# Performance work log

Measured on AMD Instinct MI355X. Metric: run time of the kernel, lower is better.

The kernel has to match this reference:

```python
import jax, jax.numpy as jnp
import numpy as np

NLAT, NLON = 256, 512
LMAX, MMAX = 256, 257  # legendre-gauss: lmax=nlat, mmax=nlon//2+1
BATCH, CHAN = 16, 8


def setup_inputs() -> dict:
    key = jax.random.key(0)
    kx, kw = jax.random.split(key)
    # vector field on the sphere: [..., 2 (theta/phi components), nlat, nlon]
    x = jax.random.normal(kx, (BATCH, CHAN, 2, NLAT, NLON), dtype=jnp.float32)
    # precomputed Legendre-derivative quadrature weights [2, mmax, lmax, nlat]
    # (stands in for precompute_dlegpoly * quad weights * 1/(l(l+1)), with weights[1] sign flip folded in)
    weights = 0.02 * jax.random.normal(kw, (2, MMAX, LMAX, NLAT), dtype=jnp.float32)
    return {"x": x, "weights": weights}


def reference(x, weights):
    # forward rfft over longitude, scaled by 2*pi (norm='forward' divides by nlon)
    xf = (2.0 * jnp.pi) * jnp.fft.rfft(x, axis=-1, norm="forward")  # [..., 2, nlat, nfreq] complex
    mmax = weights.shape[1]
    xf = xf[..., :mmax]
    # split vector components and real/imag parts
    xt = xf[..., 0, :, :]  # theta component [..., nlat, mmax]
    xp = xf[..., 1, :, :]  # phi component
    xtr, xti = jnp.real(xt), jnp.imag(xt)
    xpr, xpi = jnp.real(xp), jnp.imag(xp)
    w0 = weights[0]  # [mmax, lmax, nlat]
    w1 = weights[1]

    def contract(a, w):
        # batched per-m matmul: [..., k, m] x [m, l, k] -> [..., l, m]
        return jnp.einsum("...km,mlk->...lm", a, w)

    # spheroidal (component 0) and toroidal (component 1) coefficients
    out0 = (contract(xtr, w0) - contract(xpi, w1)) + 1j * (contract(xti, w0) + contract(xpr, w1))
    out1 = (-contract(xti, w1) - contract(xpr, w0)) + 1j * (contract(xtr, w1) - contract(xpi, w0))
    return jnp.stack([out0, out1], axis=-3)  # [..., 2, lmax, mmax] complex64
```

## Files before the change

### kernel.cpp

```cpp
#include <hip/hip_runtime.h>
#include <hip/hip_bf16.h>
#include <math.h>

#define NLAT 256
#define NLON 512
#define LMAX 256
#define MMAX 257
#define BC   128

#define X_ELEMS 33554432
#define W_ELEMS 33685504
#define W_BYTES (W_ELEMS * 4LL)

#define FM    288
#define F_BYTES  ((size_t)2*FM*512*2)
#define A_BYTES  ((size_t)4*BC*MMAX*NLAT*2)
#define OUTS_BYTES ((size_t)MMAX*2*BC*LMAX*2)

typedef short bf16x8 __attribute__((ext_vector_type(8)));
typedef float f32x4  __attribute__((ext_vector_type(4)));

__device__ __forceinline__ unsigned int bfpack2(float a, float b) {
    unsigned short lo = __builtin_bit_cast(unsigned short, __float2bfloat16(a));
    unsigned short hi = __builtin_bit_cast(unsigned short, __float2bfloat16(b));
    return (unsigned int)lo | ((unsigned int)hi << 16);
}
__device__ __forceinline__ unsigned short bf16bits(float a) {
    return __builtin_bit_cast(unsigned short, __float2bfloat16(a));
}
__device__ __forceinline__ void gload16(const void* g, void* l) {
    __builtin_amdgcn_global_load_lds(
        (const __attribute__((address_space(1))) unsigned int*)g,
        (__attribute__((address_space(3))) unsigned int*)l, 16, 0, 0);
}

__global__ __launch_bounds__(256) void f_init(unsigned short* __restrict__ F)
{
    int mm = blockIdx.x, o = blockIdx.y, t = threadIdx.x;
    const float s = 6.283185307179586f / 512.0f;
    for (int c = 0; c < 2; ++c) {
        int n = t * 2 + c;
        float val = 0.0f;
        if (mm < MMAX) {
            int j = (mm * n) & 511;
            float ang = 6.283185307179586f * (float)j / 512.0f;
            float sn, cs; __sincosf(ang, &sn, &cs);
            val = (o == 0) ? s * cs : -s * sn;
        }
        F[((size_t)o * FM + mm) * 512 + n] =
            __builtin_bit_cast(unsigned short, __float2bfloat16(val));
    }
}

__global__ __launch_bounds__(512, 1) void dft_mfma(const float* __restrict__ x,
                                                   const unsigned short* __restrict__ F,
                                                   unsigned short* __restrict__ aout)
{
    __shared__ __align__(16) unsigned char fl[2][32768];
    unsigned char* xl = (unsigned char*)fl;

    int bcc = blockIdx.x;
    int kh  = blockIdx.y;
    int bc = bcc >> 1, comp = bcc & 1;
    int t = threadIdx.x;
    int wid = t >> 6, lane = t & 63;

    int o = wid >> 2, kt = wid & 3;
    int r15 = lane & 15, hi = lane >> 4;
    int klocal = kt * 16 + r15;
    unsigned braw = (unsigned)klocal * 1024u;
    unsigned bswz = (unsigned)(klocal & 15) << 4;

    bf16x8 barr0[16], barr1[16];
    #pragma unroll
    for (int s = 0; s < 2; ++s) {
        const float* xg = x + ((size_t)bcc * NLAT + kh * 128 + s * 64) * NLON;
        #pragma unroll
        for (int p = 0; p < 8; ++p) {
            int row = wid * 8 + p;
            const float* src = xg + (size_t)row * NLON + lane * 8;
            float4 f0 = *(const float4*)(src);
            float4 f1 = *(const float4*)(src + 4);
            uint4 v;
            v.x = bfpack2(f0.x, f0.y); v.y = bfpack2(f0.z, f0.w);
            v.z = bfpack2(f1.x, f1.y); v.w = bfpack2(f1.z, f1.w);
            unsigned off = ((unsigned)row * 1024u + (unsigned)lane * 16u)
                           ^ ((unsigned)(row & 15) << 4);
            *(uint4*)(xl + off) = v;
        }
        __syncthreads();
        #pragma unroll
        for (int nt = 0; nt < 16; ++nt) {
            unsigned c0 = (unsigned)(nt * 64 + hi * 16);
            bf16x8 v = *(const bf16x8*)(xl + ((braw + c0) ^ bswz));
            if (s == 0) barr0[nt] = v; else barr1[nt] = v;
        }
        __syncthreads();
    }

    const unsigned char* Fb = (const unsigned char*)F;
    unsigned gcol = ((unsigned)lane * 16u);

    #define STAGE_F(buf, mt)                                                  \
        {                                                                     \
            _Pragma("unroll")                                                 \
            for (int p = 0; p < 4; ++p) {                                     \
                int fr = wid * 4 + p;                                         \
                int o2 = fr >> 4, mr = fr & 15;                               \
                size_t grow = (size_t)o2 * FM + (mt) * 16 + mr;               \
                const void* g = Fb + grow * 1024u                             \
                                + (gcol ^ ((unsigned)(fr & 15) << 4));        \
                gload16(g, (unsigned char*)fl[buf] + (unsigned)fr * 1024u);   \
            }                                                                 \
        }

    STAGE_F(0, 0);
    __syncthreads();

    unsigned arow = (unsigned)(o * 16 + r15);
    unsigned abase = arow * 1024u;
    unsigned aswz = (unsigned)r15 << 4;
    unsigned short* ao = aout;
    int v = comp * 2 + o;

    for (int mt = 0; mt < 17; ++mt) {
        int cur = mt & 1;
        if (mt < 16) STAGE_F(cur ^ 1, mt + 1);

        const unsigned char* fb = fl[cur];
        f32x4 accA0 = {0.f,0.f,0.f,0.f}, accA1 = {0.f,0.f,0.f,0.f};
        f32x4 accB0 = {0.f,0.f,0.f,0.f}, accB1 = {0.f,0.f,0.f,0.f};
        #pragma unroll
        for (int nt = 0; nt < 16; nt += 2) {
            unsigned c0 = (unsigned)(nt * 64 + hi * 16);
            bf16x8 a0 = *(const bf16x8*)(fb + ((abase + c0)       ^ aswz));
            bf16x8 a1 = *(const bf16x8*)(fb + ((abase + c0 + 64u) ^ aswz));
            accA0 = __builtin_amdgcn_mfma_f32_16x16x32_bf16(a0, barr0[nt],     accA0, 0, 0, 0);
            accB0 = __builtin_amdgcn_mfma_f32_16x16x32_bf16(a0, barr1[nt],     accB0, 0, 0, 0);
            accA1 = __builtin_amdgcn_mfma_f32_16x16x32_bf16(a1, barr0[nt + 1], accA1, 0, 0, 0);
            accB1 = __builtin_amdgcn_mfma_f32_16x16x32_bf16(a1, barr1[nt + 1], accB1, 0, 0, 0);
        }
        #pragma unroll
        for (int j = 0; j < 4; ++j) {
            accA0[j] += accA1[j];
            accB0[j] += accB1[j];
        }

        #pragma unroll
        for (int j = 0; j < 4; ++j) {
            int mm0 = mt * 16 + hi * 4 + j;
            if (mm0 < MMAX) {
                size_t base = (((size_t)v * BC + bc) * MMAX + mm0) * NLAT + kh * 128;
                ao[base + klocal]      = bf16bits(accA0[j]);
                ao[base + klocal + 64] = bf16bits(accB0[j]);
            }
        }
        __syncthreads();
    }
    #undef STAGE_F
}

template <int MODE>
__global__ __launch_bounds__(1024, 1) void contract_mfma(const unsigned short* __restrict__ a,
                                                         const float* __restrict__ w,
                                                         void* __restrict__ outv)
{
    __shared__ __align__(16) unsigned char Ab[2][16384];
    __shared__ __align__(16) unsigned char Bb[2][40960];
    int m  = blockIdx.x;
    int t = threadIdx.x;
    int wid = t >> 6, lane = t & 63;
    int o = wid >> 3, h = (wid >> 2) & 1, q = wid & 3;
    int r15 = lane & 15, hi = lane >> 4;

    f32x4 acc[4][4] = {};

    int pl  = t >> 9;
    int bcr = (t >> 2) & 127;
    int ch4 = t & 3;
    int lB  = t >> 2;
    int chB = t & 3;

    #define STAGE_A(buf, kt)                                                    \
        {                                                                       \
            int ph_ = (kt) >> 3;                                                \
            int k0_ = ((kt) & 7) * 32;                                          \
            int vsel = (pl == 0) ? (ph_ ? 3 : 0) : (ph_ ? 1 : 2);               \
            const void* g = a + (((size_t)vsel * BC + bcr) * MMAX + m) * NLAT   \
                              + k0_ + (ch4 ^ (bcr & 3)) * 8;                    \
            gload16(g, Ab[buf] + wid * 1024);                                   \
        }

    float4 wreg0, wreg1;
    #define WLOAD(kt)                                                           \
        {                                                                       \
            int ph_ = (kt) >> 3;                                                \
            int k0_ = ((kt) & 7) * 32;                                          \
            const float* wp = w + (((size_t)ph_ * MMAX + m) * LMAX + lB) * NLAT \
                                + k0_ + chB * 8;                                \
            wreg0 = *(const float4*)(wp);                                       \
            wreg1 = *(const float4*)(wp + 4);                                   \
        }
    #define BWRITE(buf)                                                         \
        {                                                                       \
            uint4 vv;                                                           \
            vv.x = bfpack2(wreg0.x, wreg0.y); vv.y = bfpack2(wreg0.z, wreg0.w); \
            vv.z = bfpack2(wreg1.x, wreg1.y); vv.w = bfpack2(wreg1.z, wreg1.w); \
            *(uint4*)(Bb[buf] + lB * 80 + chB * 16) = vv;                       \
            uint4 vn;                                                           \
            vn.x = vv.x ^ 0x80008000u; vn.y = vv.y ^ 0x80008000u;               \
            vn.z = vv.z ^ 0x80008000u; vn.w = vv.w ^ 0x80008000u;               \
            *(uint4*)(Bb[buf] + 20480 + lB * 80 + chB * 16) = vn;               \
        }

    STAGE_A(0, 0);
    WLOAD(0);
    __syncthreads();
    BWRITE(0);

    for (int kt2 = 0; kt2 < 16; ++kt2) {
        int cur = kt2 & 1;
        if (kt2 < 15) WLOAD(kt2 + 1);
        __syncthreads();
        if (kt2 < 15) STAGE_A(cur ^ 1, kt2 + 1);

        const unsigned char* bb = Bb[cur] + ((o == 0 && kt2 >= 8) ? 20480 : 0);
        const unsigned char* ab = Ab[cur];
        bf16x8 bfr[4];
        #pragma unroll
        for (int lt = 0; lt < 4; ++lt)
            bfr[lt] = *(const bf16x8*)(bb + (q * 64 + lt * 16 + r15) * 80 + hi * 16);
        #pragma unroll
        for (int bt = 0; bt < 4; ++bt) {
            bf16x8 af = *(const bf16x8*)(ab + (o * 128 + h * 64 + bt * 16 + r15) * 64
                                           + ((hi * 16) ^ ((r15 & 3) << 4)));
            #pragma unroll
            for (int lt = 0; lt < 4; ++lt)
                acc[bt][lt] = __builtin_amdgcn_mfma_f32_16x16x32_bf16(af, bfr[lt], acc[bt][lt], 0, 0, 0);
        }

        if (kt2 < 15) BWRITE(cur ^ 1);
    }

    #pragma unroll
    for (int bt = 0; bt < 4; ++bt) {
        #pragma unroll
        for (int lt = 0; lt < 4; ++lt) {
            #pragma unroll
            for (int j = 0; j < 4; ++j) {
                int bc = h * 64 + bt * 16 + hi * 4 + j;
                int l  = q * 64 + lt * 16 + r15;
                float av = acc[bt][lt][j];
                float val = (o == 0) ? av : (0.0f - av);
                if (MODE == 0) {
                    __hip_bfloat16* outs = (__hip_bfloat16*)outv;
                    outs[(((size_t)m * 2 + o) * BC + bc) * LMAX + l] = __float2bfloat16(val);
                } else {
                    float* out = (float*)outv;
                    out[(((size_t)bc * 2 + o) * LMAX + l) * MMAX + m] = val;
                }
            }
        }
    }
    #undef STAGE_A
    #undef WLOAD
    #undef BWRITE
}

__global__ __launch_bounds__(256) void transpose_out(const unsigned short* __restrict__ outs,
                                                     float* __restrict__ out)
{
    __shared__ float tile[32][65];
    int mt = blockIdx.x;
    int lt = blockIdx.y;
    int z  = blockIdx.z;
    int bc = z >> 1, o = z & 1;
    int t = threadIdx.x;

    {
        int r = t >> 3, c0 = (t & 7) * 8;
        int mm = mt * 32 + r;
        if (mm < MMAX) {
            const unsigned short* src = outs + (((size_t)mm * 2 + o) * BC + bc) * LMAX + lt * 64 + c0;
            uint4 v = *(const uint4*)src;
            const unsigned short* u = (const unsigned short*)&v;
            #pragma unroll
            for (int i = 0; i < 8; ++i)
                tile[r][c0 + i] = __bfloat162float(__builtin_bit_cast(__hip_bfloat16, u[i]));
        }
    }
    __syncthreads();
    {
        int l = t >> 2, mc = (t & 3) * 8;
        float* dst = out + (((size_t)bc * 2 + o) * LMAX + lt * 64 + l) * MMAX + mt * 32 + mc;
        #pragma unroll
        for (int i = 0; i < 8; ++i) {
            int mm = mt * 32 + mc + i;
            if (mm < MMAX) dst[i] = tile[mc + i][l];
        }
    }
}

#define PER_BC ((size_t)4 * MMAX * NLAT * sizeof(__hip_bfloat16))

__global__ __launch_bounds__(256) void dft_legacy(const float* __restrict__ x,
                                                  __hip_bfloat16* __restrict__ a,
                                                  int bc0, int nbc)
{
    __shared__ float  xs[512];
    __shared__ float2 tw[512];
    int t = threadIdx.x;
    int b = blockIdx.x;
    int lat = b & (NLAT - 1);
    int comp = (b >> 8) & 1;
    int bcl = b >> 9;
    int bc = bc0 + bcl;
    const float* xr = x + (((size_t)bc * 2 + comp) * NLAT + lat) * NLON;
    for (int j = t; j < 512; j += 256) {
        xs[j] = xr[j];
        float ang = -6.283185307179586f * (float)j / 512.0f;
        float sn, cs; sincosf(ang, &sn, &cs);
        tw[j] = make_float2(cs, sn);
    }
    __syncthreads();
    const float scale = 6.283185307179586f / 512.0f;
    size_t VS = (size_t)nbc * MMAX * NLAT;
    __hip_bfloat16* p0 = a + (size_t)(comp * 2) * VS + (size_t)bcl * MMAX * NLAT + lat;
    __hip_bfloat16* p1 = p0 + VS;
    for (int m = t; m < MMAX; m += 256) {
        float accr = 0.f, acci = 0.f;
        int j = 0;
        for (int n = 0; n < 512; ++n) {
            float xv = xs[n]; float2 wv = tw[j];
            accr += xv * wv.x; acci += xv * wv.y;
            j = (j + m) & 511;
        }
        p0[(size_t)m * NLAT] = __float2bfloat16(accr * scale);
        p1[(size_t)m * NLAT] = __float2bfloat16(acci * scale);
    }
}

__global__ __launch_bounds__(256) void contract_legacy(const __hip_bfloat16* __restrict__ a,
                                                       const float* __restrict__ w,
                                                       float* __restrict__ out,
                                                       int bc0, int nbc)
{
    __shared__ float w0s[16][NLAT + 1];
    __shared__ float w1s[16][NLAT + 1];
    __shared__ float as[4][4][NLAT + 1];
    __shared__ float2 red2[256];
    int tid = threadIdx.x;
    int m = blockIdx.x, l0 = blockIdx.y * 16, bct = blockIdx.z * 4;
    const float* w0g = w + ((size_t)m * LMAX + l0) * NLAT;
    const float* w1g = w0g + (size_t)MMAX * LMAX * NLAT;
    for (int idx = tid; idx < 16 * NLAT; idx += 256) {
        int l = idx >> 8, k = idx & 255;
        w0s[l][k] = w0g[(size_t)l * NLAT + k];
        w1s[l][k] = w1g[(size_t)l * NLAT + k];
    }
    size_t VS = (size_t)nbc * MMAX * NLAT;
    for (int idx = tid; idx < 4 * 4 * NLAT; idx += 256) {
        int v = idx >> 10, bl = (idx >> 8) & 3, k = idx & 255;
        int bls = bct + bl; if (bls > nbc - 1) bls = nbc - 1;
        as[v][bl][k] = __bfloat162float(a[(size_t)v * VS + ((size_t)bls * MMAX + m) * NLAT + k]);
    }
    __syncthreads();
    int l = tid & 15, b = (tid >> 4) & 3, kseg = tid >> 6;
    float acc0 = 0.f, acc2 = 0.f;
    int kbeg = kseg * 64;
    #pragma unroll 8
    for (int k = kbeg; k < kbeg + 64; ++k) {
        float tr = as[0][b][k], ti = as[1][b][k], pr = as[2][b][k], pi = as[3][b][k];
        float w0 = w0s[l][k], w1 = w1s[l][k];
        acc0 += tr * w0 - pi * w1;
        acc2 -= ti * w1 + pr * w0;
    }
    red2[tid] = make_float2(acc0, acc2);
    __syncthreads();
    if (kseg == 0 && (bct + b) < nbc) {
        #pragma unroll
        for (int s = 1; s < 4; ++s) {
            float2 r = red2[tid + 64 * s];
            acc0 += r.x; acc2 += r.y;
        }
        int bc = bc0 + bct + b;
        out[(((size_t)bc * 2 + 0) * LMAX + (l0 + l)) * MMAX + m] = acc0;
        out[(((size_t)bc * 2 + 1) * LMAX + (l0 + l)) * MMAX + m] = acc2;
    }
}

extern "C" void kernel_launch(void* const* d_in, const int* in_sizes, int n_in,
                              void* d_out, int out_size, void* d_ws, size_t ws_size,
                              hipStream_t stream)
{
    const float* x = (const float*)d_in[0];
    const float* w = (const float*)d_in[1];
    if (n_in >= 2) {
        long long s0 = (long long)in_sizes[0];
        if (s0 == (long long)W_ELEMS || s0 == W_BYTES) {
            w = (const float*)d_in[0];
            x = (const float*)d_in[1];
        }
    }
    float* out = (float*)d_out;

    if (ws_size >= F_BYTES + A_BYTES) {
        unsigned short* F = (unsigned short*)d_ws;
        unsigned short* a = (unsigned short*)((char*)d_ws + F_BYTES);
        hipLaunchKernelGGL(f_init, dim3(FM, 2), dim3(256), 0, stream, F);
        hipLaunchKernelGGL(dft_mfma, dim3(256, 2), dim3(512), 0, stream, x, F, a);
        if (ws_size >= F_BYTES + A_BYTES + OUTS_BYTES) {
            unsigned short* outs = (unsigned short*)((char*)d_ws + F_BYTES + A_BYTES);
            hipLaunchKernelGGL((contract_mfma<0>), dim3(MMAX), dim3(1024), 0, stream,
                               a, w, (void*)outs);
            hipLaunchKernelGGL(transpose_out, dim3(9, 4, 256), dim3(256), 0, stream,
                               outs, out);
        } else {
            hipLaunchKernelGGL((contract_mfma<1>), dim3(MMAX), dim3(1024), 0, stream,
                               a, w, (void*)out);
        }
    } else {
        __hip_bfloat16* a = (__hip_bfloat16*)d_ws;
        int nbc = 1;
        for (int c = 128; c >= 1; c >>= 1)
            if (PER_BC * (size_t)c <= ws_size) { nbc = c; break; }
        int nchunks = BC / nbc;
        for (int cc = 0; cc < nchunks; ++cc) {
            int bc0 = cc * nbc;
            hipLaunchKernelGGL(dft_legacy, dim3(nbc * 2 * NLAT), dim3(256), 0, stream,
                               x, a, bc0, nbc);
            hipLaunchKernelGGL(contract_legacy, dim3(MMAX, LMAX / 16, (nbc + 3) / 4),
                               dim3(256), 0, stream, a, w, out, bc0, nbc);
        }
    }
}
```

Measured before the change: 206.7 us.

## Pre-convert weights to bf16 in DFT kernel and add bf16 contraction kernel

The DFT kernel gains a tail that converts the fp32 Legendre weights to bf16 in workspace. A new contraction kernel reads those bf16 weights and splits l across two blocks per m (grid MMAX x 2, 512 threads), halving the weight bytes read in the contraction and doubling block count. The cost is an extra fp32 read plus bf16 write of the full weight tensor every call, appended to the DFT kernel. There is also some added rounding error from bf16 weights.

```diff
diff --git a/kernel.cpp b/kernel.cpp
--- a/kernel.cpp
+++ b/kernel.cpp
@@ -16,6 +16,7 @@
 #define F_BYTES  ((size_t)2*FM*512*2)
 #define A_BYTES  ((size_t)4*BC*MMAX*NLAT*2)
 #define OUTS_BYTES ((size_t)MMAX*2*BC*LMAX*2)
+#define WBF_BYTES ((size_t)W_ELEMS*2)
 
 typedef short bf16x8 __attribute__((ext_vector_type(8)));
 typedef float f32x4  __attribute__((ext_vector_type(4)));
@@ -54,7 +55,9 @@
 
 __global__ __launch_bounds__(512, 1) void dft_mfma(const float* __restrict__ x,
                                                    const unsigned short* __restrict__ F,
-                                                   unsigned short* __restrict__ aout)
+                                                   unsigned short* __restrict__ aout,
+                                                   const float* __restrict__ w,
+                                                   unsigned short* __restrict__ wbf)
 {
     __shared__ __align__(16) unsigned char fl[2][32768];
     unsigned char* xl = (unsigned char*)fl;
@@ -158,6 +161,127 @@
         __syncthreads();
     }
     #undef STAGE_F
+
+    if (wbf) {
+        int slice = bcc * 2 + kh;
+        size_t base = (size_t)slice * 65792;
+        for (int u = t; u < 8224; u += 512) {
+            size_t idx = base + (size_t)u * 8;
+            float4 f0 = *(const float4*)(w + idx);
+            float4 f1 = *(const float4*)(w + idx + 4);
+            uint4 vv;
+            vv.x = bfpack2(f0.x, f0.y); vv.y = bfpack2(f0.z, f0.w);
+            vv.z = bfpack2(f1.x, f1.y); vv.w = bfpack2(f1.z, f1.w);
+            *(uint4*)(wbf + idx) = vv;
+        }
+    }
+}
+
+template <int MODE>
+__global__ __launch_bounds__(512, 1) void contract_bf(const unsigned short* __restrict__ a,
+                                                      const unsigned short* __restrict__ wbf,
+                                                      void* __restrict__ outv)
+{
+    __shared__ __align__(16) unsigned char Ab[2][16384];
+    __shared__ __align__(16) unsigned char Bb[2][10240];
+    int m  = blockIdx.x;
+    int lh = blockIdx.y;
+    int t = threadIdx.x;
+    int wid = t >> 6, lane = t & 63;
+    int o = wid >> 2, h = (wid >> 1) & 1, q = wid & 1;
+    int r15 = lane & 15, hi = lane >> 4;
+    int l0 = lh * 128;
+
+    f32x4 accLo[4][4] = {};
+    f32x4 accHi[4][4] = {};
+
+    int bcr = t >> 2, ch4 = t & 3;
+    int lB  = t >> 2, chB = t & 3;
+
+    #define STAGE_A(buf, kt)                                                    \
+        {                                                                       \
+            int ph_ = (kt) >> 3;                                                \
+            int k0_ = ((kt) & 7) * 32;                                          \
+            _Pragma("unroll")                                                   \
+            for (int i = 0; i < 2; ++i) {                                       \
+                int vsel = (i == 0) ? (ph_ ? 3 : 0) : (ph_ ? 1 : 2);            \
+                const void* g = a + (((size_t)vsel * BC + bcr) * MMAX + m) * NLAT \
+                                  + k0_ + (ch4 ^ (bcr & 3)) * 8;                \
+                gload16(g, Ab[buf] + wid * 1024 + i * 8192);                    \
+            }                                                                   \
+        }
+
+    uint4 wvv;
+    #define WLOAD(kt)                                                           \
+        {                                                                       \
+            int ph_ = (kt) >> 3;                                                \
+            int k0_ = ((kt) & 7) * 32;                                          \
+            wvv = *(const uint4*)(wbf + (((size_t)ph_ * MMAX + m) * LMAX + l0 + lB) * NLAT \
+                                     + k0_ + chB * 8);                          \
+        }
+    #define BWRITE(buf)                                                         \
+        {                                                                       \
+            *(uint4*)(Bb[buf] + lB * 80 + chB * 16) = wvv;                      \
+        }
+    #define MFMA_PHASE(ACC)                                                     \
+        {                                                                       \
+            bf16x8 bfr[4];                                                      \
+            _Pragma("unroll")                                                   \
+            for (int lt = 0; lt < 4; ++lt)                                      \
+                bfr[lt] = *(const bf16x8*)(bb + (q * 64 + lt * 16 + r15) * 80 + hi * 16); \
+            _Pragma("unroll")                                                   \
+            for (int bt = 0; bt < 4; ++bt) {                                    \
+                bf16x8 af = *(const bf16x8*)(ab + (o * 128 + h * 64 + bt * 16 + r15) * 64 \
+                                               + ((hi * 16) ^ ((r15 & 3) << 4))); \
+                _Pragma("unroll")                                               \
+                for (int lt = 0; lt < 4; ++lt)                                  \
+                    ACC[bt][lt] = __builtin_amdgcn_mfma_f32_16x16x32_bf16(af, bfr[lt], ACC[bt][lt], 0, 0, 0); \
+            }                                                                   \
+        }
+
+    STAGE_A(0, 0);
+    WLOAD(0);
+    __syncthreads();
+    BWRITE(0);
+
+    for (int kt2 = 0; kt2 < 16; ++kt2) {
+        int cur = kt2 & 1;
+        if (kt2 < 15) WLOAD(kt2 + 1);
+        __syncthreads();
+        if (kt2 < 15) STAGE_A(cur ^ 1, kt2 + 1);
+
+        const unsigned char* bb = Bb[cur];
+        const unsigned char* ab = Ab[cur];
+        if (kt2 < 8) MFMA_PHASE(accLo) else MFMA_PHASE(accHi);
+
+        if (kt2 < 15) BWRITE(cur ^ 1);
+    }
+
+    #pragma unroll
+    for (int bt = 0; bt < 4; ++bt) {
+        #pragma unroll
+        for (int lt = 0; lt < 4; ++lt) {
+            #pragma unroll
+            for (int j = 0; j < 4; ++j) {
+                int bc = h * 64 + bt * 16 + hi * 4 + j;
+                int l  = l0 + q * 64 + lt * 16 + r15;
+                float lo = accLo[bt][lt][j];
+                float hh = accHi[bt][lt][j];
+                float val = (o == 0) ? (lo - hh) : (0.0f - (lo + hh));
+                if (MODE == 0) {
+                    __hip_bfloat16* outs = (__hip_bfloat16*)outv;
+                    outs[(((size_t)m * 2 + o) * BC + bc) * LMAX + l] = __float2bfloat16(val);
+                } else {
+                    float* out = (float*)outv;
+                    out[(((size_t)bc * 2 + o) * LMAX + l) * MMAX + m] = val;
+                }
+            }
+        }
+    }
+    #undef STAGE_A
+    #undef WLOAD
+    #undef BWRITE
+    #undef MFMA_PHASE
 }
 
 template <int MODE>
@@ -407,12 +531,22 @@
     if (ws_size >= F_BYTES + A_BYTES) {
         unsigned short* F = (unsigned short*)d_ws;
         unsigned short* a = (unsigned short*)((char*)d_ws + F_BYTES);
+        bool have_outs = ws_size >= F_BYTES + A_BYTES + OUTS_BYTES;
+        bool have_wbf  = ws_size >= F_BYTES + A_BYTES + OUTS_BYTES + WBF_BYTES;
+        unsigned short* outs = (unsigned short*)((char*)d_ws + F_BYTES + A_BYTES);
+        unsigned short* wbf  = (unsigned short*)((char*)d_ws + F_BYTES + A_BYTES + OUTS_BYTES);
+
         hipLaunchKernelGGL(f_init, dim3(FM, 2), dim3(256), 0, stream, F);
-        hipLaunchKernelGGL(dft_mfma, dim3(256, 2), dim3(512), 0, stream, x, F, a);
-        if (ws_size >= F_BYTES + A_BYTES + OUTS_BYTES) {
-            unsigned short* outs = (unsigned short*)((char*)d_ws + F_BYTES + A_BYTES);
-            hipLaunchKernelGGL((contract_mfma<0>), dim3(MMAX), dim3(1024), 0, stream,
-                               a, w, (void*)outs);
+        hipLaunchKernelGGL(dft_mfma, dim3(256, 2), dim3(512), 0, stream,
+                           x, F, a, w, have_wbf ? wbf : (unsigned short*)nullptr);
+        if (have_outs) {
+            if (have_wbf) {
+                hipLaunchKernelGGL((contract_bf<0>), dim3(MMAX, 2), dim3(512), 0, stream,
+                                   a, wbf, (void*)outs);
+            } else {
+                hipLaunchKernelGGL((contract_mfma<0>), dim3(MMAX), dim3(1024), 0, stream,
+                                   a, w, (void*)outs);
+            }
             hipLaunchKernelGGL(transpose_out, dim3(9, 4, 256), dim3(256), 0, stream,
                                outs, out);
         } else {
```

New measurement: 229.3 us. +10.9%, slower.
